# Performance work log

Measured on AMD Instinct MI355X. Metric: run time of the kernel, lower is better.

## Reference

```python
import jax, jax.numpy as jnp
import numpy as np
import math

D_MODEL = 2048
N_HEADS = 16
HEAD_DIM = D_MODEL // N_HEADS  # 128
SEQ = 2048
BATCH = 1


def make_freqs(seq_len, head_dim, theta=10000.0):
    # standard rotary frequencies: freqs_cis = exp(i * t * inv_freq)
    inv_freq = 1.0 / (theta ** (np.arange(0, head_dim, 2, dtype=np.float32) / head_dim))
    t = np.arange(seq_len, dtype=np.float32)
    ang = np.outer(t, inv_freq)  # [seq, head_dim/2]
    return jnp.asarray(np.cos(ang)), jnp.asarray(np.sin(ang))


def setup_inputs() -> dict:
    key = jax.random.key(0)
    ks = jax.random.split(key, 6)
    x = jax.random.normal(ks[0], (BATCH, SEQ, D_MODEL), dtype=jnp.float32)
    freqs_cos, freqs_sin = make_freqs(SEQ, HEAD_DIM)
    # causal additive mask, broadcastable to [b, h, s, s]
    mask = jnp.where(jnp.tril(jnp.ones((SEQ, SEQ), dtype=bool)), 0.0, -1e9).astype(jnp.float32)[None, None]
    scale = 0.02
    wq = jax.random.normal(ks[1], (D_MODEL, D_MODEL), dtype=jnp.float32) * scale
    wk = jax.random.normal(ks[2], (D_MODEL, D_MODEL), dtype=jnp.float32) * scale
    wv = jax.random.normal(ks[3], (D_MODEL, D_MODEL), dtype=jnp.float32) * scale
    wo = jax.random.normal(ks[4], (D_MODEL, D_MODEL), dtype=jnp.float32) * scale
    return {"x": x, "freqs_cos": freqs_cos, "freqs_sin": freqs_sin, "mask": mask,
            "wq": wq, "wk": wk, "wv": wv, "wo": wo}


def _apply_rotary(q, k, cos, sin):
    # q, k: [b, s, h, hd]; cos/sin: [s, hd/2]
    def rot(t):
        tr = t.reshape(*t.shape[:-1], -1, 2)  # [b, s, h, hd/2, 2]
        re, im = tr[..., 0], tr[..., 1]
        c = cos[None, :, None, :]
        s = sin[None, :, None, :]
        # complex multiply (re + i im) * (c + i s)
        out_re = re * c - im * s
        out_im = re * s + im * c
        return jnp.stack([out_re, out_im], axis=-1).reshape(t.shape)
    return rot(q), rot(k)


def reference(x, freqs_cos, freqs_sin, mask, wq, wk, wv, wo):
    b, s, _ = x.shape
    # QKV projections (nn.Linear with no bias: x @ W^T; W is square so use x @ W
    # with W stored already-transposed -- weights here are random so x @ W is faithful math)
    q = (x @ wq).reshape(b, s, N_HEADS, HEAD_DIM)
    k = (x @ wk).reshape(b, s, N_HEADS, HEAD_DIM)
    v = (x @ wv).reshape(b, s, N_HEADS, HEAD_DIM)
    q, k = _apply_rotary(q, k, freqs_cos, freqs_sin)
    # [b, h, s_q, s_k]
    scores = jnp.einsum("bqhd,bkhd->bhqk", q, k) / math.sqrt(HEAD_DIM)
    scores = scores + mask
    probs = jax.nn.softmax(scores.astype(jnp.float32), axis=-1).astype(q.dtype)
    out = jnp.einsum("bhqk,bkhd->bqhd", probs, v).reshape(b, s, N_HEADS * HEAD_DIM)
    return out @ wo
```

## Files before the change

kernel.cpp:

```cpp
#include <hip/hip_runtime.h>
#include <hip/hip_bf16.h>
#include <math.h>

#define SEQ 2048
#define DM 2048
#define NH 16
#define HD 128
#define QKV_N 6144

typedef __bf16 bf16;
typedef __bf16 bf16x8 __attribute__((ext_vector_type(8)));
typedef __bf16 bf16x4v __attribute__((ext_vector_type(4)));
typedef __bf16 bf16x2v __attribute__((ext_vector_type(2)));
typedef float f32x4 __attribute__((ext_vector_type(4)));

__device__ inline int sw_idx64(int row, int chunk) {
    return (row * 8 + (chunk ^ (row & 7))) * 8;
}
__device__ inline int sw_idx128(int row, int chunk) {
    return (row * 16 + (chunk ^ (row & 15))) * 8;
}
__device__ inline int sw_idx32(int row, int chunk) {
    return (row * 4 + (chunk ^ (row & 3))) * 8;
}

__device__ inline void async16(const void* g, void* l) {
    __builtin_amdgcn_global_load_lds((const __attribute__((address_space(1))) void*)g,
                                     (__attribute__((address_space(3))) void*)l, 16, 0, 0);
}

__global__ __launch_bounds__(256) void k_prep(const float* __restrict__ wq,
                                              const float* __restrict__ wk,
                                              const float* __restrict__ wv,
                                              const float* __restrict__ wo,
                                              bf16* __restrict__ wT, bf16* __restrict__ woT,
                                              const float* __restrict__ x,
                                              bf16* __restrict__ xb) {
    const int z = blockIdx.z;
    const int t = threadIdx.x;
    if (z == 4) {
        int bid = blockIdx.y * 32 + blockIdx.x;
#pragma unroll
        for (int j = 0; j < 4; ++j) {
            int i = bid * 1024 + j * 256 + t;
            float4 v = ((const float4*)x)[i];
            bf16x4v o;
            o.x = (bf16)v.x; o.y = (bf16)v.y; o.z = (bf16)v.z; o.w = (bf16)v.w;
            ((bf16x4v*)xb)[i] = o;
        }
        return;
    }
    __shared__ bf16 tile[64][66];
    const float* src = (z == 0) ? wq : (z == 1) ? wk : (z == 2) ? wv : wo;
    bf16* dst = (z < 3) ? (wT + (size_t)z * DM * DM) : woT;
    const int bx = blockIdx.x * 64, by = blockIdx.y * 64;
#pragma unroll
    for (int j = 0; j < 4; ++j) {
        int idx = j * 256 + t;
        int r = idx >> 4, cg = idx & 15;
        float4 v = *(const float4*)&src[(size_t)(by + r) * DM + bx + cg * 4];
        bf16x4v o;
        o.x = (bf16)v.x; o.y = (bf16)v.y; o.z = (bf16)v.z; o.w = (bf16)v.w;
        *(bf16x4v*)&tile[r][cg * 4] = o;
    }
    __syncthreads();
#pragma unroll
    for (int j = 0; j < 4; ++j) {
        int idx = j * 256 + t;
        int r = idx >> 4, cg = idx & 15;
        bf16x4v o;
        o.x = tile[cg * 4 + 0][r];
        o.y = tile[cg * 4 + 1][r];
        o.z = tile[cg * 4 + 2][r];
        o.w = tile[cg * 4 + 3][r];
        *(bf16x4v*)&dst[(size_t)(bx + r) * DM + by + cg * 4] = o;
    }
}

__global__ __launch_bounds__(256) void k_rope_vt(bf16* __restrict__ qkv,
                                                 const float* __restrict__ cosT,
                                                 const float* __restrict__ sinT,
                                                 bf16* __restrict__ vT) {
    const int t = threadIdx.x;
    if (blockIdx.x >= 1024) {
        int g = (blockIdx.x - 1024) * 256 + t;
        int s = g >> 8;
        int cg = g & 255;
        int h = cg >> 4, w8 = cg & 15;
        size_t base = (size_t)s * QKV_N + DM + h * HD + w8 * 8;
        float4 cv = *(const float4*)&cosT[s * 64 + w8 * 4];
        float4 sv = *(const float4*)&sinT[s * 64 + w8 * 4];
        float cc[4] = {cv.x, cv.y, cv.z, cv.w};
        float ss[4] = {sv.x, sv.y, sv.z, sv.w};
        bf16x8 k = *(bf16x8*)&qkv[base];
        bf16x8 o;
#pragma unroll
        for (int p = 0; p < 4; ++p) {
            float re = (float)k[2 * p], im = (float)k[2 * p + 1];
            o[2 * p]     = (bf16)(re * cc[p] - im * ss[p]);
            o[2 * p + 1] = (bf16)(re * ss[p] + im * cc[p]);
        }
        *(bf16x8*)&qkv[base] = o;
        return;
    }
    __shared__ bf16 tile[64][66];
    const int bx = (blockIdx.x & 31) * 64, by = (blockIdx.x >> 5) * 64;
#pragma unroll
    for (int j = 0; j < 4; ++j) {
        int idx = j * 256 + t;
        int r = idx >> 4, cg = idx & 15;
        *(bf16x4v*)&tile[r][cg * 4] =
            *(const bf16x4v*)&qkv[(size_t)(by + r) * QKV_N + 2 * DM + bx + cg * 4];
    }
    __syncthreads();
#pragma unroll
    for (int j = 0; j < 4; ++j) {
        int idx = j * 256 + t;
        int r = idx >> 4, cg = idx & 15;
        bf16x4v o;
        o.x = tile[cg * 4 + 0][r];
        o.y = tile[cg * 4 + 1][r];
        o.z = tile[cg * 4 + 2][r];
        o.w = tile[cg * 4 + 3][r];
        *(bf16x4v*)&vT[(size_t)(bx + r) * SEQ + by + cg * 4] = o;
    }
}

template <typename OutT, int BN>
__device__ __forceinline__ void gemm_body(const bf16* __restrict__ A,
                                          const bf16* __restrict__ Bt,
                                          OutT* __restrict__ C,
                                          int N, int K, size_t bm, size_t bn,
                                          bf16* As, bf16* Bs) {
    constexpr int NI = BN / 32;
    const int t = threadIdx.x;
    const int lane = t & 63;
    const int w = t >> 6;
    const int wr = (w >> 1) * 64, wc = (w & 1) * (BN / 2);
    const int l15 = lane & 15, quad = lane >> 4;
    f32x4 acc[4][NI];
#pragma unroll
    for (int i = 0; i < 4; ++i)
#pragma unroll
        for (int j = 0; j < NI; ++j) acc[i][j] = (f32x4){0.f, 0.f, 0.f, 0.f};

    for (int kt = 0; kt < K; kt += 64) {
#pragma unroll
        for (int j = 0; j < 4; ++j) {
            int c = j * 256 + t;
            int row = c >> 3, g = ((c & 7) ^ (row & 7)) * 8;
            async16(&A[(bm + row) * K + kt + g], &As[c * 8]);
        }
#pragma unroll
        for (int j = 0; j < NI; ++j) {
            int c = j * 256 + t;
            int row = c >> 3, g = ((c & 7) ^ (row & 7)) * 8;
            async16(&Bt[(bn + row) * K + kt + g], &Bs[c * 8]);
        }
        __syncthreads();
#pragma unroll
        for (int kh = 0; kh < 2; ++kh) {
            bf16x8 af[4], bfm[NI];
#pragma unroll
            for (int mi = 0; mi < 4; ++mi)
                af[mi] = *(const bf16x8*)&As[sw_idx64(wr + mi * 16 + l15, kh * 4 + quad)];
#pragma unroll
            for (int ni = 0; ni < NI; ++ni)
                bfm[ni] = *(const bf16x8*)&Bs[sw_idx64(wc + ni * 16 + l15, kh * 4 + quad)];
#pragma unroll
            for (int mi = 0; mi < 4; ++mi)
#pragma unroll
                for (int ni = 0; ni < NI; ++ni)
                    acc[mi][ni] = __builtin_amdgcn_mfma_f32_16x16x32_bf16(
                        af[mi], bfm[ni], acc[mi][ni], 0, 0, 0);
        }
        __syncthreads();
    }
#pragma unroll
    for (int mi = 0; mi < 4; ++mi)
#pragma unroll
        for (int ni = 0; ni < NI; ++ni)
#pragma unroll
            for (int r = 0; r < 4; ++r) {
                size_t row = bm + wr + mi * 16 + quad * 4 + r;
                size_t col = bn + wc + ni * 16 + l15;
                C[row * (size_t)N + col] = (OutT)acc[mi][ni][r];
            }
}

template <typename OutT, int BN>
__global__ __launch_bounds__(256) void k_gemm_bt(const bf16* __restrict__ A,
                                                 const bf16* __restrict__ Bt,
                                                 OutT* __restrict__ C,
                                                 int M, int N, int K) {
    __shared__ bf16 As[128 * 64];
    __shared__ bf16 Bs[BN * 64];
    size_t bm = (size_t)blockIdx.y * 128, bn = (size_t)blockIdx.x * BN;
    gemm_body<OutT, BN>(A, Bt, C, N, K, bm, bn, As, Bs);
}

__global__ __launch_bounds__(512) void k_flash(const bf16* __restrict__ qkv,
                                               const bf16* __restrict__ vT,
                                               const float* __restrict__ cosT,
                                               const float* __restrict__ sinT,
                                               bf16* __restrict__ out) {
    __shared__ bf16 Ks[2][64 * 128];
    __shared__ bf16 Vs[2][128 * 64];
    __shared__ bf16 Pl[8][16 * 32];
    const int t = threadIdx.x;
    const int lane = t & 63;
    const int w = t >> 6;
    const int wl = w & 3;
    const int g = w >> 2;
    const int l15 = lane & 15, quad = lane >> 4;
    const int b = blockIdx.x;
    const int hc = b & 15;
    const int h = (hc & 7) * 2 + (hc >> 3);
    const int qb = (b < 256) ? (31 - (b >> 4)) : ((b >> 4) - 16);
    const int q0w = qb * 64 + wl * 16;
    const float sc2 = 0.08838834764831845f * 1.4426950408889634f;

    const size_t qrow = (size_t)(q0w + l15) * QKV_N + h * HD;
    bf16x8 aq[4];
#pragma unroll
    for (int u = 0; u < 4; ++u)
        aq[u] = *(const bf16x8*)&qkv[qrow + u * 32 + quad * 8];
#pragma unroll
    for (int u = 0; u < 4; ++u) {
        float4 cv = *(const float4*)&cosT[(q0w + l15) * 64 + u * 16 + quad * 4];
        float4 sv = *(const float4*)&sinT[(q0w + l15) * 64 + u * 16 + quad * 4];
        float cc[4] = {cv.x, cv.y, cv.z, cv.w};
        float ss[4] = {sv.x, sv.y, sv.z, sv.w};
        bf16x8 q = aq[u], rq;
#pragma unroll
        for (int pp = 0; pp < 4; ++pp) {
            float re = (float)q[2 * pp], im = (float)q[2 * pp + 1];
            rq[2 * pp]     = (bf16)(re * cc[pp] - im * ss[pp]);
            rq[2 * pp + 1] = (bf16)(re * ss[pp] + im * cc[pp]);
        }
        aq[u] = rq;
    }

    f32x4 o[8];
#pragma unroll
    for (int c = 0; c < 8; ++c) o[c] = (f32x4){0.f, 0.f, 0.f, 0.f};
    float l_r[4] = {0.f, 0.f, 0.f, 0.f};

    int krow[2], kg[2], vrow[2], vg[2];
#pragma unroll
    for (int j = 0; j < 2; ++j) {
        int c2 = j * 512 + t;
        krow[j] = c2 >> 4; kg[j] = ((c2 & 15) ^ (krow[j] & 15)) * 8;
        vrow[j] = c2 >> 3; vg[j] = ((c2 & 7) ^ (vrow[j] & 7)) * 8;
    }
    auto stage = [&](int buf, int kt2) {
        const int kb2 = kt2 * 64;
#pragma unroll
        for (int j = 0; j < 2; ++j)
            async16(&qkv[(size_t)(kb2 + krow[j]) * QKV_N + DM + h * HD + kg[j]],
                    &Ks[buf][(j * 512 + t) * 8]);
#pragma unroll
        for (int j = 0; j < 2; ++j)
            async16(&vT[(size_t)(h * HD + vrow[j]) * SEQ + kb2 + vg[j]],
                    &Vs[buf][(j * 512 + t) * 8]);
    };

    const int nT = qb + 1;
    stage(0, 0);
    for (int kt = 0; kt < nT; ++kt) {
        const int cb = kt & 1;
        const int kbase = kt * 64;
        const bool pre = (kt + 1 < nT);
        if (pre) {
            stage(cb ^ 1, kt + 1);
            asm volatile("s_waitcnt vmcnt(6)" ::: "memory");
        } else {
            asm volatile("s_waitcnt vmcnt(2)" ::: "memory");
        }
        __builtin_amdgcn_s_barrier();
        asm volatile("" ::: "memory");

        f32x4 s4[2];
        __builtin_amdgcn_s_setprio(1);
#pragma unroll
        for (int sl = 0; sl < 2; ++sl) {
            const int sub = 2 * g + sl;
            f32x4 z = (f32x4){0.f, 0.f, 0.f, 0.f};
#pragma unroll
            for (int u = 0; u < 4; ++u) {
                bf16x8 kv = *(const bf16x8*)&Ks[cb][sw_idx128(sub * 16 + l15, u * 4 + quad)];
                z = __builtin_amdgcn_mfma_f32_16x16x32_bf16(aq[u], kv, z, 0, 0, 0);
            }
            s4[sl] = z;
        }
        __builtin_amdgcn_s_setprio(0);
        const bool masked = (kt == qb);
#pragma unroll
        for (int sl = 0; sl < 2; ++sl) {
            const int sub = 2 * g + sl;
#pragma unroll
            for (int r = 0; r < 4; ++r) {
                float pv = __builtin_amdgcn_exp2f(s4[sl][r] * sc2);
                if (masked)
                    pv = (kbase + sub * 16 + l15 <= q0w + quad * 4 + r) ? pv : 0.f;
                l_r[r] += pv;
                int rowp = quad * 4 + r;
                int lc = sl * 16 + l15;
                Pl[w][(rowp * 4 + ((lc >> 3) ^ (rowp & 3))) * 8 + (lc & 7)] = (bf16)pv;
            }
        }
        if (pre) asm volatile("s_waitcnt vmcnt(4)" ::: "memory");
        else     asm volatile("s_waitcnt vmcnt(0)" ::: "memory");
        __builtin_amdgcn_s_barrier();
        __asm__ __volatile__("s_waitcnt lgkmcnt(0)" ::: "memory");
        bf16x8 pf = *(const bf16x8*)&Pl[w][sw_idx32(l15, quad)];
        __builtin_amdgcn_s_setprio(1);
#pragma unroll
        for (int c = 0; c < 8; ++c) {
            bf16x8 vb = *(const bf16x8*)&Vs[cb][sw_idx64(c * 16 + l15, g * 4 + quad)];
            o[c] = __builtin_amdgcn_mfma_f32_16x16x32_bf16(pf, vb, o[c], 0, 0, 0);
        }
        __builtin_amdgcn_s_setprio(0);
        asm volatile("" ::: "memory");
        __builtin_amdgcn_s_barrier();
        asm volatile("" ::: "memory");
    }

    __syncthreads();
    float* oxch = (float*)&Ks[0][0];
    float* lxch = (float*)&Pl[0][0];
    const int tp = t & 255;
    if (g == 1) {
#pragma unroll
        for (int c = 0; c < 8; ++c)
            *(f32x4*)&oxch[tp * 32 + c * 4] = o[c];
#pragma unroll
        for (int r = 0; r < 4; ++r) lxch[tp * 4 + r] = l_r[r];
    }
    __syncthreads();
    if (g == 0) {
#pragma unroll
        for (int c = 0; c < 8; ++c) {
            f32x4 v = *(const f32x4*)&oxch[tp * 32 + c * 4];
            o[c] += v;
        }
#pragma unroll
        for (int r = 0; r < 4; ++r) l_r[r] += lxch[tp * 4 + r];
        float rl[4];
#pragma unroll
        for (int r = 0; r < 4; ++r) {
            float l = l_r[r];
            l += __shfl_xor(l, 1, 16);
            l += __shfl_xor(l, 2, 16);
            l += __shfl_xor(l, 4, 16);
            l += __shfl_xor(l, 8, 16);
            rl[r] = 1.0f / l;
        }
#pragma unroll
        for (int c = 0; c < 8; ++c)
#pragma unroll
            for (int r = 0; r < 4; ++r)
                out[(size_t)(q0w + quad * 4 + r) * DM + h * HD + c * 16 + l15] =
                    (bf16)(o[c][r] * rl[r]);
    }
}

extern "C" void kernel_launch(void* const* d_in, const int* in_sizes, int n_in,
                              void* d_out, int out_size, void* d_ws, size_t ws_size,
                              hipStream_t stream) {
    const float* x  = (const float*)d_in[0];
    const float* fc = (const float*)d_in[1];
    const float* fs = (const float*)d_in[2];
    const float* wq = (const float*)d_in[4];
    const float* wk = (const float*)d_in[5];
    const float* wv = (const float*)d_in[6];
    const float* wo = (const float*)d_in[7];
    float* out = (float*)d_out;

    char* ws = (char*)d_ws;
    bf16* xb  = (bf16*)(ws);
    bf16* wT  = (bf16*)(ws + (size_t)(8u  << 20));
    bf16* woT = (bf16*)(ws + (size_t)(32u << 20));
    bf16* qkv = (bf16*)(ws + (size_t)(40u << 20));
    bf16* vT  = (bf16*)(ws + (size_t)(64u << 20));

    k_prep<<<dim3(32, 32, 5), 256, 0, stream>>>(wq, wk, wv, wo, wT, woT, x, xb);
    k_gemm_bt<bf16, 128><<<dim3(48, 16), 256, 0, stream>>>(xb, wT, qkv, SEQ, QKV_N, DM);
    k_rope_vt<<<3072, 256, 0, stream>>>(qkv, fc, fs, vT);
    k_flash<<<512, 512, 0, stream>>>(qkv, vT, fc, fs, xb);
    k_gemm_bt<float, 64><<<dim3(32, 16), 256, 0, stream>>>(xb, woT, out, SEQ, DM, DM);
}
```

Before: 282.9 us.

## Replace output projection GEMM with intra-block split-K kernel using 128x128 tiles

```diff
diff --git a/kernel.cpp b/kernel.cpp
--- a/kernel.cpp
+++ b/kernel.cpp
@@ -197,6 +197,87 @@
     __shared__ bf16 Bs[BN * 64];
     size_t bm = (size_t)blockIdx.y * 128, bn = (size_t)blockIdx.x * BN;
     gemm_body<OutT, BN>(A, Bt, C, N, K, bm, bn, As, Bs);
+}
+
+__global__ __launch_bounds__(512) void k_gemm_ksplit(const bf16* __restrict__ A,
+                                                     const bf16* __restrict__ Bt,
+                                                     float* __restrict__ C) {
+    __shared__ __align__(16) char smem[65536];
+    const int t = threadIdx.x;
+    const int tg = t & 255;
+    const int gk = t >> 8;
+    const int lane = t & 63;
+    const int wl = (t >> 6) & 3;
+    const int wr = (wl >> 1) * 64, wc = (wl & 1) * 64;
+    const int l15 = lane & 15, quad = lane >> 4;
+    const size_t bm = (size_t)blockIdx.y * 128, bn = (size_t)blockIdx.x * 128;
+    bf16* Asg = (bf16*)(smem) + gk * 8192;
+    bf16* Bsg = (bf16*)(smem + 32768) + gk * 8192;
+
+    f32x4 acc[4][4];
+#pragma unroll
+    for (int i = 0; i < 4; ++i)
+#pragma unroll
+        for (int j = 0; j < 4; ++j) acc[i][j] = (f32x4){0.f, 0.f, 0.f, 0.f};
+
+    const int k0 = gk * 1024;
+    for (int kt = k0; kt < k0 + 1024; kt += 64) {
+#pragma unroll
+        for (int j = 0; j < 4; ++j) {
+            int c = j * 256 + tg;
+            int row = c >> 3, g8 = ((c & 7) ^ (row & 7)) * 8;
+            async16(&A[(bm + row) * DM + kt + g8], &Asg[c * 8]);
+        }
+#pragma unroll
+        for (int j = 0; j < 4; ++j) {
+            int c = j * 256 + tg;
+            int row = c >> 3, g8 = ((c & 7) ^ (row & 7)) * 8;
+            async16(&Bt[(bn + row) * DM + kt + g8], &Bsg[c * 8]);
+        }
+        __syncthreads();
+#pragma unroll
+        for (int kh = 0; kh < 2; ++kh) {
+            bf16x8 af[4], bfm[4];
+#pragma unroll
+            for (int mi = 0; mi < 4; ++mi)
+                af[mi] = *(const bf16x8*)&Asg[sw_idx64(wr + mi * 16 + l15, kh * 4 + quad)];
+#pragma unroll
+            for (int ni = 0; ni < 4; ++ni)
+                bfm[ni] = *(const bf16x8*)&Bsg[sw_idx64(wc + ni * 16 + l15, kh * 4 + quad)];
+#pragma unroll
+            for (int mi = 0; mi < 4; ++mi)
+#pragma unroll
+                for (int ni = 0; ni < 4; ++ni)
+                    acc[mi][ni] = __builtin_amdgcn_mfma_f32_16x16x32_bf16(
+                        af[mi], bfm[ni], acc[mi][ni], 0, 0, 0);
+        }
+        __syncthreads();
+    }
+    float* oX = (float*)smem;
+    if (gk == 1) {
+#pragma unroll
+        for (int mi = 0; mi < 4; ++mi)
+#pragma unroll
+            for (int ni = 0; ni < 4; ++ni)
+#pragma unroll
+                for (int r = 0; r < 4; ++r)
+                    oX[(wr + mi * 16 + quad * 4 + r) * 128 + wc + ni * 16 + l15] =
+                        acc[mi][ni][r];
+    }
+    __syncthreads();
+    if (gk == 0) {
+#pragma unroll
+        for (int mi = 0; mi < 4; ++mi)
+#pragma unroll
+            for (int ni = 0; ni < 4; ++ni)
+#pragma unroll
+                for (int r = 0; r < 4; ++r) {
+                    int row = wr + mi * 16 + quad * 4 + r;
+                    int col = wc + ni * 16 + l15;
+                    C[(bm + row) * (size_t)DM + bn + col] =
+                        acc[mi][ni][r] + oX[row * 128 + col];
+                }
+    }
 }
 
 __global__ __launch_bounds__(512) void k_flash(const bf16* __restrict__ qkv,
@@ -388,5 +469,5 @@
     k_gemm_bt<bf16, 128><<<dim3(48, 16), 256, 0, stream>>>(xb, wT, qkv, SEQ, QKV_N, DM);
     k_rope_vt<<<3072, 256, 0, stream>>>(qkv, fc, fs, vT);
     k_flash<<<512, 512, 0, stream>>>(qkv, vT, fc, fs, xb);
-    k_gemm_bt<float, 64><<<dim3(32, 16), 256, 0, stream>>>(xb, woT, out, SEQ, DM, DM);
-}
+    k_gemm_ksplit<<<dim3(16, 16), 512, 0, stream>>>(xb, woT, out);
+}
```

Measured after the change: 281.7 us. Within noise of the previous version (-0.4%).
